# Optimization experiments

Measured on AMD Instinct MI355X. Metric: run time of the kernel, lower is better.

The kernel has to match this reference:

```python
import jax, jax.numpy as jnp
import numpy as np

RATE = 2
KSIZE = 3
STRIDE = 1
SOFTMAX_SCALE = 10.0
EPS_NAN = 1e-4


def resize_bilinear_align(x, oh, ow):
    # torch F.interpolate(mode='bilinear', align_corners=True)
    B, C, H, W = x.shape
    ys = jnp.linspace(0.0, H - 1.0, oh)
    xs = jnp.linspace(0.0, W - 1.0, ow)
    y0 = jnp.floor(ys).astype(jnp.int32)
    y1 = jnp.minimum(y0 + 1, H - 1)
    wy = (ys - y0).astype(x.dtype)
    x0 = jnp.floor(xs).astype(jnp.int32)
    x1 = jnp.minimum(x0 + 1, W - 1)
    wx = (xs - x0).astype(x.dtype)
    t = x[:, :, y0, :] * (1 - wy)[None, None, :, None] + x[:, :, y1, :] * wy[None, None, :, None]
    return t[:, :, :, x0] * (1 - wx) + t[:, :, :, x1] * wx


def extract_patches(x, k, s, pad):
    # x: [C,H,W] -> [L, C, k, k] with SAME padding (pad on each side), L = oh*ow
    C, H, W = x.shape
    xp = jnp.pad(x, ((0, 0), (pad, pad), (pad, pad)))
    oh = (H + 2 * pad - k) // s + 1
    ow = (W + 2 * pad - k) // s + 1
    cols = jnp.stack(
        [xp[:, i:i + s * (oh - 1) + 1:s, j:j + s * (ow - 1) + 1:s]
         for i in range(k) for j in range(k)], axis=0)  # [k*k, C, oh, ow]
    return cols.reshape(k, k, C, oh, ow).transpose(3, 4, 2, 0, 1).reshape(oh * ow, C, k, k)


def conv2d(x, w, padding):
    # x: [N,C,H,W], w: [O,I,kh,kw]
    return jax.lax.conv_general_dilated(
        x, w, (1, 1), [(padding, padding)] * 2,
        dimension_numbers=('NCHW', 'OIHW', 'NCHW'))


def conv_transpose2d(x, w, stride, padding):
    # torch conv_transpose2d: x [N,I,h,w], w [I,O,kh,kw]
    k = w.shape[2]
    wt = jnp.flip(w, (2, 3)).transpose(1, 0, 2, 3)  # [O,I,kh,kw]
    return jax.lax.conv_general_dilated(
        x, wt, (1, 1), [(k - 1 - padding, k - 1 - padding)] * 2,
        lhs_dilation=(stride, stride),
        dimension_numbers=('NCHW', 'OIHW', 'NCHW'))


def setup_inputs() -> dict:
    key = jax.random.key(0)
    k1, k2 = jax.random.split(key)
    B, C, H, W = 4, 64, 128, 128
    background = jax.random.normal(k1, (B, C, H, W), dtype=jnp.float32)
    foreground = jax.random.normal(k2, (B, C, H, W), dtype=jnp.float32)
    return {"background": background, "foreground": foreground}


def reference(background, foreground):
    B, C, H, W = background.shape
    h, w = H // RATE, W // RATE
    fg = resize_bilinear_align(foreground, h, w)  # [B,C,h,w]
    bks = 2 * RATE  # background patch kernel = 4

    def per_sample(fg_i, bg_i):
        # foreground patches [L,C,3,3], L = h*w
        fgp = extract_patches(fg_i, KSIZE, STRIDE, 1)
        norm = jnp.sqrt(jnp.sum(fgp * fgp, axis=(1, 2, 3), keepdims=True))
        fgp_n = fgp / jnp.maximum(norm, EPS_NAN)
        # correlation score [1,L,h,w]
        score = conv2d(fg_i[None], fgp_n, padding=1)
        attn = jax.nn.softmax(score * SOFTMAX_SCALE, axis=1)
        attn = jnp.clip(attn, 1e-8, None)
        # background patches [L,C,4,4] (kernel 4, stride 2, same-pad 1)
        bgp = extract_patches(bg_i, bks, STRIDE * RATE, 1)
        out = conv_transpose2d(attn, bgp, stride=RATE, padding=1) / 4.0
        return out[0]  # [C,H,W]

    return jax.vmap(per_sample)(fg, background)
```

## Files before the change

### kernel.cpp

```cpp
#include <hip/hip_runtime.h>
#include <hip/hip_bf16.h>
#include <math.h>

#define B_  4
#define C_  64
#define H_  128
#define W_  128
#define HS  64
#define WS  64
#define L_  4096
#define K1  576
#define E2  1024
#define ZLOG (-17.5f)

typedef _Float16 f16;
typedef f16 f16x8 __attribute__((ext_vector_type(8)));
typedef float f32x4 __attribute__((ext_vector_type(4)));

__device__ __forceinline__ void gload16(const void* g, void* l) {
    __builtin_amdgcn_global_load_lds(
        (const __attribute__((address_space(1))) unsigned int*)g,
        (__attribute__((address_space(3))) unsigned int*)l, 16, 0, 0);
}

__device__ __forceinline__ int swz(int r, int c) {
    return r * 128 + ((((c >> 3) ^ (r & 7)) << 3) | (c & 7));
}

__global__ __launch_bounds__(256) void resize_kernel(const float* __restrict__ fg,
                                                     float* __restrict__ fgs) {
    int idx = blockIdx.x * 256 + threadIdx.x;
    if (idx >= B_ * C_ * HS * WS) return;
    int j = idx & 63, i = (idx >> 6) & 63, bc = idx >> 12;
    const float sc = 127.0f / 63.0f;
    float yf = i * sc, xf = j * sc;
    int y0 = (int)floorf(yf); if (y0 > 127) y0 = 127;
    int x0 = (int)floorf(xf); if (x0 > 127) x0 = 127;
    int y1 = min(y0 + 1, 127), x1 = min(x0 + 1, 127);
    float wy = yf - (float)y0, wx = xf - (float)x0;
    const float* p = fg + (size_t)bc * (H_ * W_);
    float a = p[y0 * W_ + x0], b = p[y0 * W_ + x1];
    float c = p[y1 * W_ + x0], d = p[y1 * W_ + x1];
    float t0 = a * (1.f - wy) + c * wy;
    float t1 = b * (1.f - wy) + d * wy;
    fgs[idx] = t0 * (1.f - wx) + t1 * wx;
}

__global__ __launch_bounds__(256) void patch_kernel(const float* __restrict__ fgs,
                                                    f16* __restrict__ P_all,
                                                    float* __restrict__ nrmsq) {
    int idx = blockIdx.x * 256 + threadIdx.x;
    int b = blockIdx.y;
    int k = idx % K1, l = idx / K1;
    int c = k / 9, r = k % 9;
    int dy = r / 3, dx = r % 3;
    int ly = l >> 6, lx = l & 63;
    int y = ly - 1 + dy, x = lx - 1 + dx;
    float v = 0.f;
    if ((unsigned)y < 64u && (unsigned)x < 64u)
        v = fgs[((size_t)b * C_ + c) * (HS * WS) + y * WS + x];
    P_all[(size_t)b * L_ * K1 + idx] = (f16)v;
    float s = v * v;
    #pragma unroll
    for (int off = 32; off; off >>= 1) s += __shfl_down(s, off);
    if ((threadIdx.x & 63) == 0) atomicAdd(&nrmsq[b * L_ + l], s);
}

__global__ __launch_bounds__(256) void v_kernel(const float* __restrict__ bg_g,
                                                f16* __restrict__ VT_g) {
    int ls = blockIdx.y;
    const float* bg_b = bg_g + (size_t)ls * (C_ * H_ * W_);
    f16* VT = VT_g + (size_t)ls * ((size_t)E2 * L_);
    int idx = blockIdx.x * 256 + threadIdx.x;
    int l = idx & 4095, e = idx >> 12;
    int c = e >> 4, r = e & 15;
    int ky = r >> 2, kx = r & 3;
    int ly = l >> 6, lx = l & 63;
    int by = 2 * ly - 1 + ky, bx = 2 * lx - 1 + kx;
    float v = 0.f;
    if ((unsigned)by < 128u && (unsigned)bx < 128u)
        v = bg_b[(size_t)c * (H_ * W_) + by * W_ + bx];
    VT[idx] = (f16)v;
}

__device__ __forceinline__ int nextk(int kn, int kLen, unsigned long long mask) {
    while (kn < kLen) {
        int t = kn >> 7;
        if (mask & (1ull << t)) return kn;
        unsigned long long m = mask >> t;
        if (!m) return kLen;
        kn = (t + __builtin_ctzll(m)) << 7;
    }
    return kn;
}

template <int EPI>
__global__ __launch_bounds__(512, 4)
void mfma_gemm(const f16* __restrict__ A, size_t sA,
               const f16* __restrict__ Bt, size_t sB,
               int lda, int ldb, int kLen, void* __restrict__ outp, size_t sOut,
               int ldc, const float* __restrict__ nrm, float* __restrict__ rowsum,
               int* __restrict__ flags) {
    __shared__ __align__(16) f16 As[2][2][128 * 32];
    __shared__ __align__(16) f16 Bs[2][2][128 * 32];
    __shared__ float sred[16];

    const int lin = blockIdx.x;
    const int S = gridDim.x >> 3;
    int bx, by, ls;
    if (EPI == 1) {
        int s = (lin & 7) * S + (lin >> 3);
        int R = s / 136, q = s - R * 136;
        ls = R >> 2;
        int rr = R & 3;
        if (rr < 2) {
            int a = 0;
            while (q >= 16 - a) { q -= 16 - a; ++a; }
            by = a + (rr << 4); bx = a + q + (rr << 4);
        } else {
            if (q >= 128) return;
            by = q & 15; bx = 16 + ((rr & 1) << 3) + (q >> 4);
        }
    } else {
        int G = (lin & 7) * S + (lin >> 3);
        ls = G >> 8;
        by = (G >> 5) & 7; bx = G & 31;
    }

    A  += (size_t)ls * sA;
    Bt += (size_t)ls * sB;
    f16* outbase = (f16*)outp + (size_t)ls * sOut;
    if (EPI == 1) { nrm += (size_t)ls * L_; rowsum += (size_t)ls * L_; }
    flags += ls * 1024;

    const int tid = threadIdx.x;
    const int w = tid >> 6, lane = tid & 63;
    const int row0 = by * 128, col0 = bx * 128;

    unsigned long long kmask = ~0ull;
    if (EPI == 0) {
        int f = (lane < 32) ? flags[bx * 32 + lane] : 0;
        kmask = __ballot(f != 0);
    }

    const int srow = tid >> 2;
    const int scol = (((tid & 3) ^ ((tid >> 3) & 3)) * 8);
    const f16* gA = A + (size_t)(row0 + srow) * lda + scol;
    const f16* gB = Bt + (size_t)(col0 + srow) * ldb + scol;
    const int ld = tid * 8;

    const int wm = w >> 2, wn = w & 3;
    const int mfm = lane & 15, quad = lane >> 4;
    const int rq = (quad ^ ((mfm >> 1) & 3)) * 8;
    f32x4 acc[4][2] = {};

    int kc = (EPI == 0) ? nextk(0, kLen, kmask) : 0;
    if (kc < kLen) {
        int cur = 0;
        gload16(gA + kc,      &As[0][0][ld]);
        gload16(gA + kc + 32, &As[0][1][ld]);
        gload16(gB + kc,      &Bs[0][0][ld]);
        gload16(gB + kc + 32, &Bs[0][1][ld]);
        for (;;) {
            int kn = (EPI == 0) ? nextk(kc + 64, kLen, kmask) : kc + 64;
            __builtin_amdgcn_s_barrier();
            if (kn < kLen) {
                const int nxt = cur ^ 1;
                gload16(gA + kn,      &As[nxt][0][ld]);
                gload16(gA + kn + 32, &As[nxt][1][ld]);
                gload16(gB + kn,      &Bs[nxt][0][ld]);
                gload16(gB + kn + 32, &Bs[nxt][1][ld]);
                asm volatile("s_waitcnt vmcnt(4)" ::: "memory");
            } else {
                asm volatile("s_waitcnt vmcnt(0)" ::: "memory");
            }
            __builtin_amdgcn_s_barrier();
            __builtin_amdgcn_sched_barrier(0);
            #pragma unroll
            for (int h = 0; h < 2; ++h) {
                f16x8 af[4], bf[2];
                #pragma unroll
                for (int mi = 0; mi < 4; ++mi)
                    af[mi] = *(const f16x8*)&As[cur][h][(wm * 64 + mi * 16 + mfm) * 32 + rq];
                #pragma unroll
                for (int ni = 0; ni < 2; ++ni)
                    bf[ni] = *(const f16x8*)&Bs[cur][h][(wn * 32 + ni * 16 + mfm) * 32 + rq];
                #pragma unroll
                for (int mi = 0; mi < 4; ++mi)
                    #pragma unroll
                    for (int ni = 0; ni < 2; ++ni)
                        acc[mi][ni] = __builtin_amdgcn_mfma_f32_16x16x32_f16(
                            af[mi], bf[ni], acc[mi][ni], 0, 0, 0);
            }
            cur ^= 1;
            kc = kn;
            if (kc >= kLen) break;
        }
    }

    const int orow = row0 + wm * 64;
    const int ocol = col0 + wn * 32;
    f16* st = &As[0][0][0];

    if (EPI == 1) {
        f16* Eo = outbase;
        const bool offd = (by != bx);
        float rowm[16], csr[16], cs[2], cm2[2];
        #pragma unroll
        for (int j = 0; j < 16; ++j) {
            float n = fmaxf(sqrtf(nrm[orow + (j >> 2) * 16 + quad * 4 + (j & 3)]), 1e-4f);
            rowm[j] = 10.0f * n; csr[j] = 10.0f / n;
        }
        #pragma unroll
        for (int ni = 0; ni < 2; ++ni) {
            float n = fmaxf(sqrtf(nrm[ocol + ni * 16 + mfm]), 1e-4f);
            cs[ni] = 10.0f / n; cm2[ni] = 10.0f * n;
        }
        float mx1 = -1e30f, mx2 = -1e30f;
        #pragma unroll
        for (int ni = 0; ni < 2; ++ni)
            #pragma unroll
            for (int mi = 0; mi < 4; ++mi)
                #pragma unroll
                for (int r = 0; r < 4; ++r) {
                    float a = acc[mi][ni][r];
                    mx1 = fmaxf(mx1, a * cs[ni] - rowm[mi * 4 + r]);
                    mx2 = fmaxf(mx2, a * csr[mi * 4 + r] - cm2[ni]);
                }
        #pragma unroll
        for (int off = 32; off; off >>= 1) {
            mx1 = fmaxf(mx1, __shfl_xor(mx1, off));
            mx2 = fmaxf(mx2, __shfl_xor(mx2, off));
        }
        if (lane == 0) { sred[w] = mx1; sred[8 + w] = mx2; }
        __syncthreads();
        float b1 = sred[0], b2 = sred[8];
        #pragma unroll
        for (int k = 1; k < 8; ++k) {
            b1 = fmaxf(b1, sred[k]); b2 = fmaxf(b2, sred[8 + k]);
        }
        int nz1 = b1 > ZLOG;
        int nz2 = offd && (b2 > ZLOG);
        if (nz1) {
            float rs[16] = {};
            #pragma unroll
            for (int ni = 0; ni < 2; ++ni)
                #pragma unroll
                for (int mi = 0; mi < 4; ++mi)
                    #pragma unroll
                    for (int r = 0; r < 4; ++r) {
                        float e = __expf(acc[mi][ni][r] * cs[ni] - rowm[mi * 4 + r]);
                        rs[mi * 4 + r] += e;
                        st[swz(wm * 64 + mi * 16 + quad * 4 + r,
                               wn * 32 + ni * 16 + mfm)] = (f16)e;
                    }
            __syncthreads();
            #pragma unroll
            for (int it = 0; it < 4; ++it) {
                int chunk = it * 512 + tid;
                int row = chunk >> 4, c16 = chunk & 15;
                f16x8 v = *(const f16x8*)&st[row * 128 + ((c16 ^ (row & 7)) << 3)];
                *(f16x8*)&Eo[(size_t)(row0 + row) * ldc + col0 + c16 * 8] = v;
            }
            #pragma unroll
            for (int j = 0; j < 16; ++j) {
                float v = rs[j];
                v += __shfl_xor(v, 1); v += __shfl_xor(v, 2);
                v += __shfl_xor(v, 4); v += __shfl_xor(v, 8);
                if (mfm == 0)
                    atomicAdd(&rowsum[orow + (j >> 2) * 16 + quad * 4 + (j & 3)], v);
            }
        }
        if (nz2) {
            __syncthreads();
            float rs2[2] = {};
            #pragma unroll
            for (int ni = 0; ni < 2; ++ni)
                #pragma unroll
                for (int mi = 0; mi < 4; ++mi)
                    #pragma unroll
                    for (int r = 0; r < 4; ++r) {
                        float e = __expf(acc[mi][ni][r] * csr[mi * 4 + r] - cm2[ni]);
                        rs2[ni] += e;
                        st[swz(wn * 32 + ni * 16 + mfm,
                               wm * 64 + mi * 16 + quad * 4 + r)] = (f16)e;
                    }
            __syncthreads();
            #pragma unroll
            for (int it = 0; it < 4; ++it) {
                int chunk = it * 512 + tid;
                int row = chunk >> 4, c16 = chunk & 15;
                f16x8 v = *(const f16x8*)&st[row * 128 + ((c16 ^ (row & 7)) << 3)];
                *(f16x8*)&Eo[(size_t)(col0 + row) * ldc + row0 + c16 * 8] = v;
            }
            #pragma unroll
            for (int ni = 0; ni < 2; ++ni) {
                float v = rs2[ni];
                v += __shfl_xor(v, 16); v += __shfl_xor(v, 32);
                if (quad == 0)
                    atomicAdd(&rowsum[ocol + ni * 16 + mfm], v);
            }
        }
        if (tid == 0) {
            flags[by * 32 + bx] = nz1;
            if (offd) flags[bx * 32 + by] = nz2;
        }
    } else {
        __syncthreads();
        #pragma unroll
        for (int ni = 0; ni < 2; ++ni)
            #pragma unroll
            for (int mi = 0; mi < 4; ++mi)
                #pragma unroll
                for (int r = 0; r < 4; ++r)
                    st[swz(wm * 64 + mi * 16 + quad * 4 + r,
                           wn * 32 + ni * 16 + mfm)] = (f16)acc[mi][ni][r];
        __syncthreads();
        f16* base = outbase + (size_t)row0 * ldc + col0;
        #pragma unroll
        for (int it = 0; it < 4; ++it) {
            int chunk = it * 512 + tid;
            int row = chunk >> 4, c16 = chunk & 15;
            f16x8 v = *(const f16x8*)&st[row * 128 + ((c16 ^ (row & 7)) << 3)];
            *(f16x8*)&base[(size_t)row * ldc + c16 * 8] = v;
        }
    }
}

__global__ __launch_bounds__(256) void gather_kernel(const f16* __restrict__ OPT_g,
                                                     const float* __restrict__ rowsum_g,
                                                     float* __restrict__ out_g) {
    int ls = blockIdx.y;
    const f16* OPT = OPT_g + (size_t)ls * ((size_t)E2 * L_);
    const float* rowsum = rowsum_g + (size_t)ls * L_;
    float* out_b = out_g + (size_t)ls * (C_ * H_ * W_);
    int idx = blockIdx.x * 256 + threadIdx.x;
    if (idx >= C_ * H_ * W_) return;
    int X = idx & 127, Y = (idx >> 7) & 127, c = idx >> 14;
    int kyp = (Y + 1) & 1;
    int kxp = (X + 1) & 1;
    float sum = 0.f;
    #pragma unroll
    for (int ky = kyp; ky < 4; ky += 2) {
        int py = (Y + 1 - ky) >> 1;
        if ((unsigned)py >= 64u) continue;
        #pragma unroll
        for (int kx = kxp; kx < 4; kx += 2) {
            int px = (X + 1 - kx) >> 1;
            if ((unsigned)px >= 64u) continue;
            int p = py * 64 + px;
            int e = c * 16 + ky * 4 + kx;
            float v = (float)OPT[(size_t)e * L_ + p];
            sum += v * __builtin_amdgcn_rcpf(rowsum[p]);
        }
    }
    out_b[idx] = 0.25f * sum;
}

extern "C" void kernel_launch(void* const* d_in, const int* in_sizes, int n_in,
                              void* d_out, int out_size, void* d_ws, size_t ws_size,
                              hipStream_t stream) {
    const float* bg = (const float*)d_in[0];
    const float* fg = (const float*)d_in[1];
    float* out = (float*)d_out;
    char* w8 = (char*)d_ws;

    float* fgs        = (float*)(w8);
    f16*   P_all      = (f16*)  (w8 + 4194304);
    float* nrmsq      = (float*)(w8 + 23068672);
    float* rowsum_all = (float*)(w8 + 23134208);
    int*   flags      = (int*)  (w8 + 23199744);
    const size_t base = 23216128;

    const size_t EB_ELEMS = (size_t)L_ * L_;
    f16* Eb_all  = (f16*)(w8 + base);
    f16* VT_all  = (f16*)(w8 + base + 4 * EB_ELEMS * 2);
    f16* OPT_all = (f16*)w8;

    hipMemsetAsync(nrmsq, 0, 131072, stream);

    resize_kernel<<<(B_ * C_ * HS * WS) / 256, 256, 0, stream>>>(fg, fgs);
    patch_kernel<<<dim3((L_ * K1) / 256, B_), 256, 0, stream>>>(fgs, P_all, nrmsq);

    mfma_gemm<1><<<2176, 512, 0, stream>>>(
        P_all, (size_t)L_ * K1, P_all, (size_t)L_ * K1,
        K1, K1, K1, Eb_all, EB_ELEMS, L_,
        nrmsq, rowsum_all, flags);

    for (int g = 0; g < B_; g += 2) {
        v_kernel<<<dim3((L_ * E2) / 256, 2), 256, 0, stream>>>(
            bg + (size_t)g * C_ * H_ * W_, VT_all);

        mfma_gemm<0><<<512, 512, 0, stream>>>(
            VT_all, (size_t)E2 * L_, Eb_all + (size_t)g * EB_ELEMS, EB_ELEMS,
            L_, L_, L_, OPT_all, (size_t)E2 * L_, L_,
            nullptr, nullptr, flags + g * 1024);

        gather_kernel<<<dim3((C_ * H_ * W_) / 256, 2), 256, 0, stream>>>(
            OPT_all, rowsum_all + (size_t)g * L_, out + (size_t)g * C_ * H_ * W_);
    }
}
```

Before: 249.1 us.

## Fuse all stages into one persistent cooperative kernel with grid syncs

Replaces the memset and the separate resize, patch, GEMM, value-build and gather launches with a single cooperative persistent kernel. The stages are separated by grid-wide barriers and GEMM tiles are walked in grid-stride loops. The aim is to remove per-launch overhead and the gaps between kernels. In exchange the grid is capped at 256 or 512 blocks, so the GEMM stages get less parallelism than the original 2176 and 512-block launches. The kernel also adds grid sync costs and a host occupancy query on every call.

```diff
diff --git a/kernel.cpp b/kernel.cpp
--- a/kernel.cpp
+++ b/kernel.cpp
@@ -1,6 +1,9 @@
 #include <hip/hip_runtime.h>
+#include <hip/hip_cooperative_groups.h>
 #include <hip/hip_bf16.h>
 #include <math.h>
+
+namespace cg = cooperative_groups;
 
 #define B_  4
 #define C_  64
@@ -27,62 +30,6 @@
     return r * 128 + ((((c >> 3) ^ (r & 7)) << 3) | (c & 7));
 }
 
-__global__ __launch_bounds__(256) void resize_kernel(const float* __restrict__ fg,
-                                                     float* __restrict__ fgs) {
-    int idx = blockIdx.x * 256 + threadIdx.x;
-    if (idx >= B_ * C_ * HS * WS) return;
-    int j = idx & 63, i = (idx >> 6) & 63, bc = idx >> 12;
-    const float sc = 127.0f / 63.0f;
-    float yf = i * sc, xf = j * sc;
-    int y0 = (int)floorf(yf); if (y0 > 127) y0 = 127;
-    int x0 = (int)floorf(xf); if (x0 > 127) x0 = 127;
-    int y1 = min(y0 + 1, 127), x1 = min(x0 + 1, 127);
-    float wy = yf - (float)y0, wx = xf - (float)x0;
-    const float* p = fg + (size_t)bc * (H_ * W_);
-    float a = p[y0 * W_ + x0], b = p[y0 * W_ + x1];
-    float c = p[y1 * W_ + x0], d = p[y1 * W_ + x1];
-    float t0 = a * (1.f - wy) + c * wy;
-    float t1 = b * (1.f - wy) + d * wy;
-    fgs[idx] = t0 * (1.f - wx) + t1 * wx;
-}
-
-__global__ __launch_bounds__(256) void patch_kernel(const float* __restrict__ fgs,
-                                                    f16* __restrict__ P_all,
-                                                    float* __restrict__ nrmsq) {
-    int idx = blockIdx.x * 256 + threadIdx.x;
-    int b = blockIdx.y;
-    int k = idx % K1, l = idx / K1;
-    int c = k / 9, r = k % 9;
-    int dy = r / 3, dx = r % 3;
-    int ly = l >> 6, lx = l & 63;
-    int y = ly - 1 + dy, x = lx - 1 + dx;
-    float v = 0.f;
-    if ((unsigned)y < 64u && (unsigned)x < 64u)
-        v = fgs[((size_t)b * C_ + c) * (HS * WS) + y * WS + x];
-    P_all[(size_t)b * L_ * K1 + idx] = (f16)v;
-    float s = v * v;
-    #pragma unroll
-    for (int off = 32; off; off >>= 1) s += __shfl_down(s, off);
-    if ((threadIdx.x & 63) == 0) atomicAdd(&nrmsq[b * L_ + l], s);
-}
-
-__global__ __launch_bounds__(256) void v_kernel(const float* __restrict__ bg_g,
-                                                f16* __restrict__ VT_g) {
-    int ls = blockIdx.y;
-    const float* bg_b = bg_g + (size_t)ls * (C_ * H_ * W_);
-    f16* VT = VT_g + (size_t)ls * ((size_t)E2 * L_);
-    int idx = blockIdx.x * 256 + threadIdx.x;
-    int l = idx & 4095, e = idx >> 12;
-    int c = e >> 4, r = e & 15;
-    int ky = r >> 2, kx = r & 3;
-    int ly = l >> 6, lx = l & 63;
-    int by = 2 * ly - 1 + ky, bx = 2 * lx - 1 + kx;
-    float v = 0.f;
-    if ((unsigned)by < 128u && (unsigned)bx < 128u)
-        v = bg_b[(size_t)c * (H_ * W_) + by * W_ + bx];
-    VT[idx] = (f16)v;
-}
-
 __device__ __forceinline__ int nextk(int kn, int kLen, unsigned long long mask) {
     while (kn < kLen) {
         int t = kn >> 7;
@@ -95,44 +42,14 @@
 }
 
 template <int EPI>
-__global__ __launch_bounds__(512, 4)
-void mfma_gemm(const f16* __restrict__ A, size_t sA,
-               const f16* __restrict__ Bt, size_t sB,
-               int lda, int ldb, int kLen, void* __restrict__ outp, size_t sOut,
-               int ldc, const float* __restrict__ nrm, float* __restrict__ rowsum,
-               int* __restrict__ flags) {
-    __shared__ __align__(16) f16 As[2][2][128 * 32];
-    __shared__ __align__(16) f16 Bs[2][2][128 * 32];
-    __shared__ float sred[16];
-
-    const int lin = blockIdx.x;
-    const int S = gridDim.x >> 3;
-    int bx, by, ls;
-    if (EPI == 1) {
-        int s = (lin & 7) * S + (lin >> 3);
-        int R = s / 136, q = s - R * 136;
-        ls = R >> 2;
-        int rr = R & 3;
-        if (rr < 2) {
-            int a = 0;
-            while (q >= 16 - a) { q -= 16 - a; ++a; }
-            by = a + (rr << 4); bx = a + q + (rr << 4);
-        } else {
-            if (q >= 128) return;
-            by = q & 15; bx = 16 + ((rr & 1) << 3) + (q >> 4);
-        }
-    } else {
-        int G = (lin & 7) * S + (lin >> 3);
-        ls = G >> 8;
-        by = (G >> 5) & 7; bx = G & 31;
-    }
-
-    A  += (size_t)ls * sA;
-    Bt += (size_t)ls * sB;
-    f16* outbase = (f16*)outp + (size_t)ls * sOut;
-    if (EPI == 1) { nrm += (size_t)ls * L_; rowsum += (size_t)ls * L_; }
-    flags += ls * 1024;
-
+__device__ __forceinline__ void gemm_slot(
+    int by, int bx,
+    const f16* __restrict__ A, const f16* __restrict__ Bt,
+    int lda, int ldb, int kLen, f16* __restrict__ outbase, int ldc,
+    const float* __restrict__ nrm, float* __restrict__ rowsum,
+    int* __restrict__ flags,
+    f16* __restrict__ AsB, f16* __restrict__ BsB, float* __restrict__ sred)
+{
     const int tid = threadIdx.x;
     const int w = tid >> 6, lane = tid & 63;
     const int row0 = by * 128, col0 = bx * 128;
@@ -157,19 +74,19 @@
     int kc = (EPI == 0) ? nextk(0, kLen, kmask) : 0;
     if (kc < kLen) {
         int cur = 0;
-        gload16(gA + kc,      &As[0][0][ld]);
-        gload16(gA + kc + 32, &As[0][1][ld]);
-        gload16(gB + kc,      &Bs[0][0][ld]);
-        gload16(gB + kc + 32, &Bs[0][1][ld]);
+        gload16(gA + kc,      AsB + ld);
+        gload16(gA + kc + 32, AsB + 4096 + ld);
+        gload16(gB + kc,      BsB + ld);
+        gload16(gB + kc + 32, BsB + 4096 + ld);
         for (;;) {
             int kn = (EPI == 0) ? nextk(kc + 64, kLen, kmask) : kc + 64;
             __builtin_amdgcn_s_barrier();
             if (kn < kLen) {
                 const int nxt = cur ^ 1;
-                gload16(gA + kn,      &As[nxt][0][ld]);
-                gload16(gA + kn + 32, &As[nxt][1][ld]);
-                gload16(gB + kn,      &Bs[nxt][0][ld]);
-                gload16(gB + kn + 32, &Bs[nxt][1][ld]);
+                gload16(gA + kn,      AsB + nxt * 8192 + ld);
+                gload16(gA + kn + 32, AsB + nxt * 8192 + 4096 + ld);
+                gload16(gB + kn,      BsB + nxt * 8192 + ld);
+                gload16(gB + kn + 32, BsB + nxt * 8192 + 4096 + ld);
                 asm volatile("s_waitcnt vmcnt(4)" ::: "memory");
             } else {
                 asm volatile("s_waitcnt vmcnt(0)" ::: "memory");
@@ -178,13 +95,15 @@
             __builtin_amdgcn_sched_barrier(0);
             #pragma unroll
             for (int h = 0; h < 2; ++h) {
+                const f16* Ab = AsB + cur * 8192 + h * 4096;
+                const f16* Bb = BsB + cur * 8192 + h * 4096;
                 f16x8 af[4], bf[2];
                 #pragma unroll
                 for (int mi = 0; mi < 4; ++mi)
-                    af[mi] = *(const f16x8*)&As[cur][h][(wm * 64 + mi * 16 + mfm) * 32 + rq];
+                    af[mi] = *(const f16x8*)&Ab[(wm * 64 + mi * 16 + mfm) * 32 + rq];
                 #pragma unroll
                 for (int ni = 0; ni < 2; ++ni)
-                    bf[ni] = *(const f16x8*)&Bs[cur][h][(wn * 32 + ni * 16 + mfm) * 32 + rq];
+                    bf[ni] = *(const f16x8*)&Bb[(wn * 32 + ni * 16 + mfm) * 32 + rq];
                 #pragma unroll
                 for (int mi = 0; mi < 4; ++mi)
                     #pragma unroll
@@ -200,7 +119,7 @@
 
     const int orow = row0 + wm * 64;
     const int ocol = col0 + wn * 32;
-    f16* st = &As[0][0][0];
+    f16* st = AsB;
 
     if (EPI == 1) {
         f16* Eo = outbase;
@@ -325,36 +244,156 @@
             *(f16x8*)&base[(size_t)row * ldc + c16 * 8] = v;
         }
     }
-}
-
-__global__ __launch_bounds__(256) void gather_kernel(const f16* __restrict__ OPT_g,
-                                                     const float* __restrict__ rowsum_g,
-                                                     float* __restrict__ out_g) {
-    int ls = blockIdx.y;
-    const f16* OPT = OPT_g + (size_t)ls * ((size_t)E2 * L_);
-    const float* rowsum = rowsum_g + (size_t)ls * L_;
-    float* out_b = out_g + (size_t)ls * (C_ * H_ * W_);
-    int idx = blockIdx.x * 256 + threadIdx.x;
-    if (idx >= C_ * H_ * W_) return;
-    int X = idx & 127, Y = (idx >> 7) & 127, c = idx >> 14;
-    int kyp = (Y + 1) & 1;
-    int kxp = (X + 1) & 1;
-    float sum = 0.f;
-    #pragma unroll
-    for (int ky = kyp; ky < 4; ky += 2) {
-        int py = (Y + 1 - ky) >> 1;
-        if ((unsigned)py >= 64u) continue;
-        #pragma unroll
-        for (int kx = kxp; kx < 4; kx += 2) {
-            int px = (X + 1 - kx) >> 1;
-            if ((unsigned)px >= 64u) continue;
-            int p = py * 64 + px;
-            int e = c * 16 + ky * 4 + kx;
-            float v = (float)OPT[(size_t)e * L_ + p];
-            sum += v * __builtin_amdgcn_rcpf(rowsum[p]);
-        }
-    }
-    out_b[idx] = 0.25f * sum;
+    __syncthreads();
+}
+
+__global__ __launch_bounds__(512, 4)
+void mega_kernel(const float* __restrict__ bg, const float* __restrict__ fg,
+                 float* __restrict__ out, char* __restrict__ w8)
+{
+    __shared__ __align__(16) f16 AsB[2 * 2 * 4096];
+    __shared__ __align__(16) f16 BsB[2 * 2 * 4096];
+    __shared__ float sred[16];
+
+    cg::grid_group gg = cg::this_grid();
+    const int NT = gridDim.x * 512;
+    const int gtid = blockIdx.x * 512 + threadIdx.x;
+
+    float* fgs        = (float*)(w8);
+    f16*   P_all      = (f16*)  (w8 + 4194304);
+    float* nrmsq      = (float*)(w8 + 23068672);
+    float* rowsum_all = (float*)(w8 + 23134208);
+    int*   flags      = (int*)  (w8 + 23199744);
+    const size_t EB = (size_t)L_ * L_;
+    f16* Eb_all  = (f16*)(w8 + 23216128);
+    f16* VT_all  = (f16*)(w8 + 23216128 + 4 * EB * 2);
+    f16* OPT_all = (f16*)w8;
+
+    for (int i = gtid; i < 32768; i += NT) nrmsq[i] = 0.f;
+    for (int idx = gtid; idx < B_ * C_ * HS * WS; idx += NT) {
+        int j = idx & 63, i = (idx >> 6) & 63, bc = idx >> 12;
+        const float sc = 127.0f / 63.0f;
+        float yf = i * sc, xf = j * sc;
+        int y0 = (int)floorf(yf); if (y0 > 127) y0 = 127;
+        int x0 = (int)floorf(xf); if (x0 > 127) x0 = 127;
+        int y1 = min(y0 + 1, 127), x1 = min(x0 + 1, 127);
+        float wy = yf - (float)y0, wx = xf - (float)x0;
+        const float* p = fg + (size_t)bc * (H_ * W_);
+        float a = p[y0 * W_ + x0], b = p[y0 * W_ + x1];
+        float c = p[y1 * W_ + x0], d = p[y1 * W_ + x1];
+        float t0 = a * (1.f - wy) + c * wy;
+        float t1 = b * (1.f - wy) + d * wy;
+        fgs[idx] = t0 * (1.f - wx) + t1 * wx;
+    }
+    __threadfence();
+    gg.sync();
+
+    for (int idx = gtid; idx < B_ * L_ * K1; idx += NT) {
+        int b = idx / (L_ * K1);
+        int rem = idx - b * (L_ * K1);
+        int k = rem % K1, l = rem / K1;
+        int c = k / 9, r = k % 9;
+        int dy = r / 3, dx = r % 3;
+        int ly = l >> 6, lx = l & 63;
+        int y = ly - 1 + dy, x = lx - 1 + dx;
+        float v = 0.f;
+        if ((unsigned)y < 64u && (unsigned)x < 64u)
+            v = fgs[((size_t)b * C_ + c) * (HS * WS) + y * WS + x];
+        P_all[idx] = (f16)v;
+        float s = v * v;
+        #pragma unroll
+        for (int off = 32; off; off >>= 1) s += __shfl_down(s, off);
+        if ((threadIdx.x & 63) == 0) atomicAdd(&nrmsq[b * L_ + l], s);
+    }
+    __threadfence();
+    gg.sync();
+
+    {
+        const int xcd = blockIdx.x & 7, bi = blockIdx.x >> 3;
+        const int bpx = gridDim.x >> 3;
+        for (int qx = bi; qx < 272; qx += bpx) {
+            int s = xcd * 272 + qx;
+            int R = s / 136, q = s - R * 136;
+            int ls = R >> 2, rr = R & 3, by = 0, bx = 0;
+            bool ok = true;
+            if (rr < 2) {
+                int a = 0;
+                while (q >= 16 - a) { q -= 16 - a; ++a; }
+                by = a + (rr << 4); bx = a + q + (rr << 4);
+            } else {
+                if (q >= 128) ok = false;
+                else { by = q & 15; bx = 16 + ((rr & 1) << 3) + (q >> 4); }
+            }
+            if (ok)
+                gemm_slot<1>(by, bx,
+                    P_all + (size_t)ls * L_ * K1, P_all + (size_t)ls * L_ * K1,
+                    K1, K1, K1, Eb_all + (size_t)ls * EB, L_,
+                    nrmsq + (size_t)ls * L_, rowsum_all + (size_t)ls * L_,
+                    flags + ls * 1024, AsB, BsB, sred);
+        }
+    }
+    __threadfence();
+    gg.sync();
+
+    for (int g = 0; g < B_; g += 2) {
+        for (int idx = gtid; idx < 2 * E2 * L_; idx += NT) {
+            int lsv = idx >> 22, rem = idx & 4194303;
+            int l = rem & 4095, e = rem >> 12;
+            int c = e >> 4, r = e & 15;
+            int ky = r >> 2, kx = r & 3;
+            int ly = l >> 6, lx = l & 63;
+            int byy = 2 * ly - 1 + ky, bxx = 2 * lx - 1 + kx;
+            float v = 0.f;
+            if ((unsigned)byy < 128u && (unsigned)bxx < 128u)
+                v = bg[(size_t)(g + lsv) * (C_ * H_ * W_) +
+                       (size_t)c * (H_ * W_) + byy * W_ + bxx];
+            VT_all[idx] = (f16)v;
+        }
+        __threadfence();
+        gg.sync();
+
+        {
+            const int xcd = blockIdx.x & 7, bi = blockIdx.x >> 3;
+            const int bpx = gridDim.x >> 3;
+            for (int qx = bi; qx < 64; qx += bpx) {
+                int G = xcd * 64 + qx;
+                int ls = G >> 8;
+                int by = (G >> 5) & 7, bx = G & 31;
+                gemm_slot<0>(by, bx,
+                    VT_all + (size_t)ls * E2 * L_,
+                    Eb_all + (size_t)(g + ls) * EB,
+                    L_, L_, L_, OPT_all + (size_t)ls * E2 * L_, L_,
+                    nullptr, nullptr, flags + (g + ls) * 1024, AsB, BsB, sred);
+            }
+        }
+        __threadfence();
+        gg.sync();
+
+        for (int idx = gtid; idx < 2 * C_ * H_ * W_; idx += NT) {
+            int lsg = idx >> 20, rem = idx & 1048575;
+            int X = rem & 127, Y = (rem >> 7) & 127, c = rem >> 14;
+            const f16* OPT = OPT_all + (size_t)lsg * E2 * L_;
+            const float* rowsum = rowsum_all + (size_t)(g + lsg) * L_;
+            int kyp = (Y + 1) & 1, kxp = (X + 1) & 1;
+            float sum = 0.f;
+            #pragma unroll
+            for (int ky = kyp; ky < 4; ky += 2) {
+                int py = (Y + 1 - ky) >> 1;
+                if ((unsigned)py >= 64u) continue;
+                #pragma unroll
+                for (int kx = kxp; kx < 4; kx += 2) {
+                    int px = (X + 1 - kx) >> 1;
+                    if ((unsigned)px >= 64u) continue;
+                    int p = py * 64 + px;
+                    int e = c * 16 + ky * 4 + kx;
+                    float v = (float)OPT[(size_t)e * L_ + p];
+                    sum += v * __builtin_amdgcn_rcpf(rowsum[p]);
+                }
+            }
+            out[(size_t)(g + lsg) * (C_ * H_ * W_) + rem] = 0.25f * sum;
+        }
+        if (g + 2 < B_) { __threadfence(); gg.sync(); }
+    }
 }
 
 extern "C" void kernel_launch(void* const* d_in, const int* in_sizes, int n_in,
@@ -365,38 +404,10 @@
     float* out = (float*)d_out;
     char* w8 = (char*)d_ws;
 
-    float* fgs        = (float*)(w8);
-    f16*   P_all      = (f16*)  (w8 + 4194304);
-    float* nrmsq      = (float*)(w8 + 23068672);
-    float* rowsum_all = (float*)(w8 + 23134208);
-    int*   flags      = (int*)  (w8 + 23199744);
-    const size_t base = 23216128;
-
-    const size_t EB_ELEMS = (size_t)L_ * L_;
-    f16* Eb_all  = (f16*)(w8 + base);
-    f16* VT_all  = (f16*)(w8 + base + 4 * EB_ELEMS * 2);
-    f16* OPT_all = (f16*)w8;
-
-    hipMemsetAsync(nrmsq, 0, 131072, stream);
-
-    resize_kernel<<<(B_ * C_ * HS * WS) / 256, 256, 0, stream>>>(fg, fgs);
-    patch_kernel<<<dim3((L_ * K1) / 256, B_), 256, 0, stream>>>(fgs, P_all, nrmsq);
-
-    mfma_gemm<1><<<2176, 512, 0, stream>>>(
-        P_all, (size_t)L_ * K1, P_all, (size_t)L_ * K1,
-        K1, K1, K1, Eb_all, EB_ELEMS, L_,
-        nrmsq, rowsum_all, flags);
-
-    for (int g = 0; g < B_; g += 2) {
-        v_kernel<<<dim3((L_ * E2) / 256, 2), 256, 0, stream>>>(
-            bg + (size_t)g * C_ * H_ * W_, VT_all);
-
-        mfma_gemm<0><<<512, 512, 0, stream>>>(
-            VT_all, (size_t)E2 * L_, Eb_all + (size_t)g * EB_ELEMS, EB_ELEMS,
-            L_, L_, L_, OPT_all, (size_t)E2 * L_, L_,
-            nullptr, nullptr, flags + g * 1024);
-
-        gather_kernel<<<dim3((C_ * H_ * W_) / 256, 2), 256, 0, stream>>>(
-            OPT_all, rowsum_all + (size_t)g * L_, out + (size_t)g * C_ * H_ * W_);
-    }
-}
+    int maxb = 0;
+    hipOccupancyMaxActiveBlocksPerMultiprocessor(&maxb, mega_kernel, 512, 0);
+    int grid = (maxb >= 2) ? 512 : 256;
+
+    void* args[] = { (void*)&bg, (void*)&fg, (void*)&out, (void*)&w8 };
+    hipLaunchCooperativeKernel(mega_kernel, dim3(grid), dim3(512), args, 0, stream);
+}
```

Measured after the change: 894.6 us. 3.59x slower.

## Overlap background patch build and gather with GEMM launches via block specialization

Applied to the files above, without the earlier changes.

Extra thread blocks are appended to the score GEMM so they build the first background-patch matrix while the GEMM runs. A combined kernel builds the second pair's patch matrix and gathers the first pair's output in the same launch. The patch build now writes 8 halves per vector store, and the norm-buffer memset moves into the resize kernel. The goal is fewer launches and less idle tail time between stages, at the cost of the extra blocks competing with the GEMM for compute units.

```diff
diff --git a/kernel.cpp b/kernel.cpp
--- a/kernel.cpp
+++ b/kernel.cpp
@@ -27,9 +27,75 @@
     return r * 128 + ((((c >> 3) ^ (r & 7)) << 3) | (c & 7));
 }
 
+__device__ __forceinline__ int nextk(int kn, int kLen, unsigned long long mask) {
+    while (kn < kLen) {
+        int t = kn >> 7;
+        if (mask & (1ull << t)) return kn;
+        unsigned long long m = mask >> t;
+        if (!m) return kLen;
+        kn = (t + __builtin_ctzll(m)) << 7;
+    }
+    return kn;
+}
+
+__device__ __forceinline__ void vbuild_pair(const float* __restrict__ bg2,
+                                            f16* __restrict__ VT, int t, int nthr) {
+    const int nvec = (2 * E2 * L_) / 8;
+    for (int v = t; v < nvec; v += nthr) {
+        int gidx = v << 3;
+        int lsv = gidx >> 22, rem = gidx & 4194303;
+        int e = rem >> 12, l0 = rem & 4095;
+        int c = e >> 4, r = e & 15, ky = r >> 2, kx = r & 3;
+        int ly = l0 >> 6, lx0 = l0 & 63;
+        int byy = 2 * ly - 1 + ky;
+        const float* row = bg2 + (size_t)lsv * (C_ * H_ * W_)
+                               + (size_t)c * (H_ * W_) + byy * W_;
+        f16x8 o;
+        #pragma unroll
+        for (int i = 0; i < 8; ++i) {
+            int bxx = 2 * (lx0 + i) - 1 + kx;
+            float val = 0.f;
+            if ((unsigned)byy < 128u && (unsigned)bxx < 128u) val = row[bxx];
+            o[i] = (f16)val;
+        }
+        *(f16x8*)&VT[gidx] = o;
+    }
+}
+
+__device__ __forceinline__ void gather_pair(const f16* __restrict__ OPT_g,
+                                            const float* __restrict__ rowsum_g,
+                                            float* __restrict__ out_g,
+                                            int t, int nthr) {
+    for (int idx = t; idx < 2 * C_ * H_ * W_; idx += nthr) {
+        int lsg = idx >> 20, rem = idx & 1048575;
+        int X = rem & 127, Y = (rem >> 7) & 127, c = rem >> 14;
+        const f16* OPT = OPT_g + (size_t)lsg * ((size_t)E2 * L_);
+        const float* rowsum = rowsum_g + (size_t)lsg * L_;
+        int kyp = (Y + 1) & 1, kxp = (X + 1) & 1;
+        float sum = 0.f;
+        #pragma unroll
+        for (int ky = kyp; ky < 4; ky += 2) {
+            int py = (Y + 1 - ky) >> 1;
+            if ((unsigned)py >= 64u) continue;
+            #pragma unroll
+            for (int kx = kxp; kx < 4; kx += 2) {
+                int px = (X + 1 - kx) >> 1;
+                if ((unsigned)px >= 64u) continue;
+                int p = py * 64 + px;
+                int e = c * 16 + ky * 4 + kx;
+                float v = (float)OPT[(size_t)e * L_ + p];
+                sum += v * __builtin_amdgcn_rcpf(rowsum[p]);
+            }
+        }
+        out_g[(size_t)lsg * (C_ * H_ * W_) + rem] = 0.25f * sum;
+    }
+}
+
 __global__ __launch_bounds__(256) void resize_kernel(const float* __restrict__ fg,
-                                                     float* __restrict__ fgs) {
+                                                     float* __restrict__ fgs,
+                                                     float* __restrict__ nrmsq) {
     int idx = blockIdx.x * 256 + threadIdx.x;
+    if (idx < 32768) nrmsq[idx] = 0.f;
     if (idx >= B_ * C_ * HS * WS) return;
     int j = idx & 63, i = (idx >> 6) & 63, bc = idx >> 12;
     const float sc = 127.0f / 63.0f;
@@ -66,32 +132,19 @@
     if ((threadIdx.x & 63) == 0) atomicAdd(&nrmsq[b * L_ + l], s);
 }
 
-__global__ __launch_bounds__(256) void v_kernel(const float* __restrict__ bg_g,
-                                                f16* __restrict__ VT_g) {
-    int ls = blockIdx.y;
-    const float* bg_b = bg_g + (size_t)ls * (C_ * H_ * W_);
-    f16* VT = VT_g + (size_t)ls * ((size_t)E2 * L_);
-    int idx = blockIdx.x * 256 + threadIdx.x;
-    int l = idx & 4095, e = idx >> 12;
-    int c = e >> 4, r = e & 15;
-    int ky = r >> 2, kx = r & 3;
-    int ly = l >> 6, lx = l & 63;
-    int by = 2 * ly - 1 + ky, bx = 2 * lx - 1 + kx;
-    float v = 0.f;
-    if ((unsigned)by < 128u && (unsigned)bx < 128u)
-        v = bg_b[(size_t)c * (H_ * W_) + by * W_ + bx];
-    VT[idx] = (f16)v;
-}
-
-__device__ __forceinline__ int nextk(int kn, int kLen, unsigned long long mask) {
-    while (kn < kLen) {
-        int t = kn >> 7;
-        if (mask & (1ull << t)) return kn;
-        unsigned long long m = mask >> t;
-        if (!m) return kLen;
-        kn = (t + __builtin_ctzll(m)) << 7;
-    }
-    return kn;
+__global__ __launch_bounds__(512) void gv_kernel(const float* __restrict__ bg2,
+                                                 f16* __restrict__ VT,
+                                                 const f16* __restrict__ OPT_g,
+                                                 const float* __restrict__ rowsum_g,
+                                                 float* __restrict__ out_g,
+                                                 int nvb) {
+    if (blockIdx.x < nvb) {
+        vbuild_pair(bg2, VT, blockIdx.x * 512 + threadIdx.x, nvb * 512);
+    } else {
+        gather_pair(OPT_g, rowsum_g, out_g,
+                    (blockIdx.x - nvb) * 512 + threadIdx.x,
+                    (gridDim.x - nvb) * 512);
+    }
 }
 
 template <int EPI>
@@ -100,13 +153,20 @@
                const f16* __restrict__ Bt, size_t sB,
                int lda, int ldb, int kLen, void* __restrict__ outp, size_t sOut,
                int ldc, const float* __restrict__ nrm, float* __restrict__ rowsum,
-               int* __restrict__ flags) {
+               int* __restrict__ flags,
+               const float* __restrict__ vbg, f16* __restrict__ vdst, int ngemm) {
     __shared__ __align__(16) f16 As[2][2][128 * 32];
     __shared__ __align__(16) f16 Bs[2][2][128 * 32];
     __shared__ float sred[16];
 
     const int lin = blockIdx.x;
-    const int S = gridDim.x >> 3;
+    if (lin >= ngemm) {
+        vbuild_pair(vbg, vdst, (lin - ngemm) * 512 + threadIdx.x,
+                    (gridDim.x - ngemm) * 512);
+        return;
+    }
+
+    const int S = ngemm >> 3;
     int bx, by, ls;
     if (EPI == 1) {
         int s = (lin & 7) * S + (lin >> 3);
@@ -327,36 +387,6 @@
     }
 }
 
-__global__ __launch_bounds__(256) void gather_kernel(const f16* __restrict__ OPT_g,
-                                                     const float* __restrict__ rowsum_g,
-                                                     float* __restrict__ out_g) {
-    int ls = blockIdx.y;
-    const f16* OPT = OPT_g + (size_t)ls * ((size_t)E2 * L_);
-    const float* rowsum = rowsum_g + (size_t)ls * L_;
-    float* out_b = out_g + (size_t)ls * (C_ * H_ * W_);
-    int idx = blockIdx.x * 256 + threadIdx.x;
-    if (idx >= C_ * H_ * W_) return;
-    int X = idx & 127, Y = (idx >> 7) & 127, c = idx >> 14;
-    int kyp = (Y + 1) & 1;
-    int kxp = (X + 1) & 1;
-    float sum = 0.f;
-    #pragma unroll
-    for (int ky = kyp; ky < 4; ky += 2) {
-        int py = (Y + 1 - ky) >> 1;
-        if ((unsigned)py >= 64u) continue;
-        #pragma unroll
-        for (int kx = kxp; kx < 4; kx += 2) {
-            int px = (X + 1 - kx) >> 1;
-            if ((unsigned)px >= 64u) continue;
-            int p = py * 64 + px;
-            int e = c * 16 + ky * 4 + kx;
-            float v = (float)OPT[(size_t)e * L_ + p];
-            sum += v * __builtin_amdgcn_rcpf(rowsum[p]);
-        }
-    }
-    out_b[idx] = 0.25f * sum;
-}
-
 extern "C" void kernel_launch(void* const* d_in, const int* in_sizes, int n_in,
                               void* d_out, int out_size, void* d_ws, size_t ws_size,
                               hipStream_t stream) {
@@ -377,26 +407,32 @@
     f16* VT_all  = (f16*)(w8 + base + 4 * EB_ELEMS * 2);
     f16* OPT_all = (f16*)w8;
 
-    hipMemsetAsync(nrmsq, 0, 131072, stream);
-
-    resize_kernel<<<(B_ * C_ * HS * WS) / 256, 256, 0, stream>>>(fg, fgs);
+    const size_t CHW = (size_t)C_ * H_ * W_;
+
+    resize_kernel<<<(B_ * C_ * HS * WS) / 256, 256, 0, stream>>>(fg, fgs, nrmsq);
     patch_kernel<<<dim3((L_ * K1) / 256, B_), 256, 0, stream>>>(fgs, P_all, nrmsq);
 
-    mfma_gemm<1><<<2176, 512, 0, stream>>>(
+    mfma_gemm<1><<<2176 + 512, 512, 0, stream>>>(
         P_all, (size_t)L_ * K1, P_all, (size_t)L_ * K1,
         K1, K1, K1, Eb_all, EB_ELEMS, L_,
-        nrmsq, rowsum_all, flags);
-
-    for (int g = 0; g < B_; g += 2) {
-        v_kernel<<<dim3((L_ * E2) / 256, 2), 256, 0, stream>>>(
-            bg + (size_t)g * C_ * H_ * W_, VT_all);
-
-        mfma_gemm<0><<<512, 512, 0, stream>>>(
-            VT_all, (size_t)E2 * L_, Eb_all + (size_t)g * EB_ELEMS, EB_ELEMS,
-            L_, L_, L_, OPT_all, (size_t)E2 * L_, L_,
-            nullptr, nullptr, flags + g * 1024);
-
-        gather_kernel<<<dim3((C_ * H_ * W_) / 256, 2), 256, 0, stream>>>(
-            OPT_all, rowsum_all + (size_t)g * L_, out + (size_t)g * C_ * H_ * W_);
-    }
-}
+        nrmsq, rowsum_all, flags,
+        bg, VT_all, 2176);
+
+    mfma_gemm<0><<<512, 512, 0, stream>>>(
+        VT_all, (size_t)E2 * L_, Eb_all, EB_ELEMS,
+        L_, L_, L_, OPT_all, (size_t)E2 * L_, L_,
+        nullptr, nullptr, flags,
+        nullptr, nullptr, 512);
+
+    gv_kernel<<<512 + 1024, 512, 0, stream>>>(
+        bg + 2 * CHW, VT_all, OPT_all, rowsum_all, out, 512);
+
+    mfma_gemm<0><<<512, 512, 0, stream>>>(
+        VT_all, (size_t)E2 * L_, Eb_all + 2 * EB_ELEMS, EB_ELEMS,
+        L_, L_, L_, OPT_all, (size_t)E2 * L_, L_,
+        nullptr, nullptr, flags + 2 * 1024,
+        nullptr, nullptr, 512);
+
+    gv_kernel<<<1024, 512, 0, stream>>>(
+        nullptr, nullptr, OPT_all, rowsum_all + 2 * L_, out + 2 * CHW, 0);
+}
```

Measured after the change: 246.0 us. No clear change (-1.2%).
